# Optimization experiments

Hardware: AMD Instinct MI355X
Metric: run time of the kernel (lower is better)

Reference implementation:

```python
import jax, jax.numpy as jnp
import numpy as np

N_SAMPLES = 8388608  # total packed samples across all rays
N_RAYS = 131072      # number of rays (segments)


def setup_inputs() -> dict:
    key = jax.random.key(0)
    k1, k2, k3 = jax.random.split(key, 3)
    # Sorted segment ids emulate the packed ray layout (samples of a ray are contiguous).
    segment_ids = jnp.sort(
        jax.random.randint(k1, (N_SAMPLES,), 0, N_RAYS, dtype=jnp.int32)
    )
    rgb_samples = jax.random.normal(k2, (N_SAMPLES, 3), dtype=jnp.float32)
    weights_samples = jax.random.uniform(k3, (N_SAMPLES, 1), dtype=jnp.float32)
    return {
        "segment_ids": segment_ids,
        "rgb_samples": rgb_samples,
        "weights_samples": weights_samples,
        "n_rays": N_RAYS,
    }


def reference(segment_ids, rgb_samples, weights_samples, n_rays):
    # pred_rgb[r] = sum over samples s belonging to ray r of w_s * rgb_s
    weighted = rgb_samples * weights_samples  # [N,3], weight broadcast over channels
    pred_rgb = jax.ops.segment_sum(weighted, segment_ids, num_segments=n_rays)  # [n_rays,3]
    return pred_rgb
```

## Files before the change

kernel.cpp:

```cpp
#include <hip/hip_runtime.h>


__global__ __launch_bounds__(256) void find_starts_kernel(
    const int* __restrict__ ids, int n_samples, int n_rays,
    int* __restrict__ starts) {
  int i = blockIdx.x * blockDim.x + threadIdx.x;
  if (i >= n_samples) return;
  int b = ids[i];
  int a = (i == 0) ? -1 : ids[i - 1];
  for (int r = a + 1; r <= b; ++r) starts[r] = i;
  if (i == n_samples - 1) {
    for (int r = b + 1; r <= n_rays; ++r) starts[r] = n_samples;
  }
}

__global__ __launch_bounds__(256) void reduce_rays_kernel(
    const float* __restrict__ rgb, const float* __restrict__ w,
    const int* __restrict__ starts, float* __restrict__ out, int n_rays) {
  int gtid = blockIdx.x * blockDim.x + threadIdx.x;
  int ray = gtid >> 6;
  int lane = threadIdx.x & 63;
  if (ray >= n_rays) return;
  int s0 = starts[ray];
  int s1 = starts[ray + 1];
  float r = 0.f, g = 0.f, b = 0.f;
  for (int s = s0 + lane; s < s1; s += 64) {
    float ww = w[s];
    r += ww * rgb[3 * s + 0];
    g += ww * rgb[3 * s + 1];
    b += ww * rgb[3 * s + 2];
  }
  for (int off = 32; off; off >>= 1) {
    r += __shfl_down(r, off, 64);
    g += __shfl_down(g, off, 64);
    b += __shfl_down(b, off, 64);
  }
  if (lane == 0) {
    out[3 * ray + 0] = r;
    out[3 * ray + 1] = g;
    out[3 * ray + 2] = b;
  }
}

extern "C" void kernel_launch(void* const* d_in, const int* in_sizes, int n_in,
                              void* d_out, int out_size, void* d_ws, size_t ws_size,
                              hipStream_t stream) {
  const int*   segment_ids = (const int*)d_in[0];
  const float* rgb         = (const float*)d_in[1];
  const float* weights     = (const float*)d_in[2];
  float*       out         = (float*)d_out;

  const int n_samples = in_sizes[0];
  const int n_rays    = out_size / 3;

  int* starts = (int*)d_ws;

  {
    int threads = 256;
    int blocks = (n_samples + threads - 1) / threads;
    find_starts_kernel<<<blocks, threads, 0, stream>>>(
        segment_ids, n_samples, n_rays, starts);
  }
  {
    int threads = 256;
    long long total_threads = (long long)n_rays * 64;
    int blocks = (int)((total_threads + threads - 1) / threads);
    reduce_rays_kernel<<<blocks, threads, 0, stream>>>(
        rgb, weights, starts, out, n_rays);
  }
}
```

Measured before the change: 207.9 us.

## Vectorize boundary detection and coalesce RGB loads with shuffle-broadcast weights

find_starts now loads four segment ids per thread through int4 and takes the previous id from a neighbouring lane by warp shuffle. The reduction walks each ray's RGB data as a flat float stream, so consecutive lanes read consecutive floats instead of stride-3 addresses. Each lane's weight is broadcast to the matching channel lanes with __shfl, and lane%3 decides which accumulator belongs to which channel. The intent is fully coalesced loads in both kernels, at the cost of extra shuffles and slightly more involved channel bookkeeping.

```diff
diff --git a/kernel.cpp b/kernel.cpp
--- a/kernel.cpp
+++ b/kernel.cpp
@@ -4,41 +4,85 @@
 __global__ __launch_bounds__(256) void find_starts_kernel(
     const int* __restrict__ ids, int n_samples, int n_rays,
     int* __restrict__ starts) {
-  int i = blockIdx.x * blockDim.x + threadIdx.x;
-  if (i >= n_samples) return;
-  int b = ids[i];
-  int a = (i == 0) ? -1 : ids[i - 1];
-  for (int r = a + 1; r <= b; ++r) starts[r] = i;
-  if (i == n_samples - 1) {
-    for (int r = b + 1; r <= n_rays; ++r) starts[r] = n_samples;
+  int i4 = blockIdx.x * blockDim.x + threadIdx.x;
+  int base = i4 * 4;
+  if (base >= n_samples) return;
+  int lane = threadIdx.x & 63;
+
+  int4 v;
+  if (base + 3 < n_samples) {
+    v = ((const int4*)ids)[i4];
+  } else {
+    v.x = ids[base];
+    v.y = (base + 1 < n_samples) ? ids[base + 1] : v.x;
+    v.z = (base + 2 < n_samples) ? ids[base + 2] : v.y;
+    v.w = (base + 3 < n_samples) ? ids[base + 3] : v.z;
+  }
+  int prev = __shfl_up(v.w, 1, 64);
+  if (lane == 0) prev = (base == 0) ? -1 : ids[base - 1];
+
+  int a[5] = {prev, v.x, v.y, v.z, v.w};
+  #pragma unroll
+  for (int t = 0; t < 4; ++t) {
+    int hi = (base + t < n_samples) ? a[t + 1] : a[t];
+    for (int r = a[t] + 1; r <= hi; ++r) starts[r] = base + t;
+  }
+  if (base + 4 >= n_samples) {
+    int last = a[4];
+    for (int r = last + 1; r <= n_rays; ++r) starts[r] = n_samples;
   }
 }
 
 __global__ __launch_bounds__(256) void reduce_rays_kernel(
     const float* __restrict__ rgb, const float* __restrict__ w,
     const int* __restrict__ starts, float* __restrict__ out, int n_rays) {
-  int gtid = blockIdx.x * blockDim.x + threadIdx.x;
-  int ray = gtid >> 6;
   int lane = threadIdx.x & 63;
+  int ray = __builtin_amdgcn_readfirstlane(
+      blockIdx.x * (blockDim.x >> 6) + (threadIdx.x >> 6));
   if (ray >= n_rays) return;
   int s0 = starts[ray];
   int s1 = starts[ray + 1];
-  float r = 0.f, g = 0.f, b = 0.f;
-  for (int s = s0 + lane; s < s1; s += 64) {
-    float ww = w[s];
-    r += ww * rgb[3 * s + 0];
-    g += ww * rgb[3 * s + 1];
-    b += ww * rgb[3 * s + 2];
+  int L  = s1 - s0;
+  int nf = 3 * L;
+  const float* __restrict__ rgbf = rgb + 3 * (long long)s0;
+  const float* __restrict__ wseg = w + s0;
+
+  float acc0 = 0.f, acc1 = 0.f, acc2 = 0.f;
+  for (int k = 0; 192 * k < nf; ++k) {
+    int si = 64 * k + lane;
+    float wv = (si < L) ? wseg[si] : 0.f;
+    {
+      int e = 192 * k + lane;
+      float rv = (e < nf) ? rgbf[e] : 0.f;
+      acc0 += rv * __shfl(wv, lane / 3, 64);
+    }
+    {
+      int e = 192 * k + 64 + lane;
+      float rv = (e < nf) ? rgbf[e] : 0.f;
+      acc1 += rv * __shfl(wv, (64 + lane) / 3, 64);
+    }
+    {
+      int e = 192 * k + 128 + lane;
+      float rv = (e < nf) ? rgbf[e] : 0.f;
+      acc2 += rv * __shfl(wv, (128 + lane) / 3, 64);
+    }
   }
+
+  int m = lane % 3;
+  float c0 = (m == 0) ? acc0 : (m == 1) ? acc2 : acc1;
+  float c1 = (m == 0) ? acc1 : (m == 1) ? acc0 : acc2;
+  float c2 = (m == 0) ? acc2 : (m == 1) ? acc1 : acc0;
+
+  #pragma unroll
   for (int off = 32; off; off >>= 1) {
-    r += __shfl_down(r, off, 64);
-    g += __shfl_down(g, off, 64);
-    b += __shfl_down(b, off, 64);
+    c0 += __shfl_down(c0, off, 64);
+    c1 += __shfl_down(c1, off, 64);
+    c2 += __shfl_down(c2, off, 64);
   }
   if (lane == 0) {
-    out[3 * ray + 0] = r;
-    out[3 * ray + 1] = g;
-    out[3 * ray + 2] = b;
+    out[3 * ray + 0] = c0;
+    out[3 * ray + 1] = c1;
+    out[3 * ray + 2] = c2;
   }
 }
 
@@ -57,14 +101,14 @@
 
   {
     int threads = 256;
-    int blocks = (n_samples + threads - 1) / threads;
+    int elems4  = (n_samples + 3) / 4;
+    int blocks  = (elems4 + threads - 1) / threads;
     find_starts_kernel<<<blocks, threads, 0, stream>>>(
         segment_ids, n_samples, n_rays, starts);
   }
   {
     int threads = 256;
-    long long total_threads = (long long)n_rays * 64;
-    int blocks = (int)((total_threads + threads - 1) / threads);
+    int blocks  = (n_rays + 3) / 4;
     reduce_rays_kernel<<<blocks, threads, 0, stream>>>(
         rgb, weights, starts, out, n_rays);
   }
```

Measured after the change: 208.2 us. About the same (+0.1%).

## Replace start-index search and per-ray wave reduction with chunked LDS segmented accumulation

Applied to the files above, without the earlier changes.

Drops the two-pass scheme, which first built ray start offsets and then used one 64-lane wave per ray. Each block now processes a contiguous chunk of 1024 samples with vectorized float4 loads. Each thread merges runs of equal ids in registers, accumulates them into an LDS buffer with LDS atomics, and then writes interior rays directly and boundary rays with global atomics after a zeroing pass. This removes the starts workspace traffic and the poor lane utilization when rays hold only about 64 samples. In exchange it relies on float atomics, so summation order is nondeterministic, and it needs a separate kernel to zero the output. The leftover-element branch in the zeroing code is empty.

```diff
diff --git a/kernel.cpp b/kernel.cpp
--- a/kernel.cpp
+++ b/kernel.cpp
@@ -1,44 +1,125 @@
 #include <hip/hip_runtime.h>
 
 
-__global__ __launch_bounds__(256) void find_starts_kernel(
-    const int* __restrict__ ids, int n_samples, int n_rays,
-    int* __restrict__ starts) {
+#define CHUNK    1024
+#define CAP      1024
+#define NTHREADS 256
+
+__global__ __launch_bounds__(NTHREADS) void zero_out_kernel(float4* __restrict__ out4,
+                                                            int n4) {
   int i = blockIdx.x * blockDim.x + threadIdx.x;
-  if (i >= n_samples) return;
-  int b = ids[i];
-  int a = (i == 0) ? -1 : ids[i - 1];
-  for (int r = a + 1; r <= b; ++r) starts[r] = i;
-  if (i == n_samples - 1) {
-    for (int r = b + 1; r <= n_rays; ++r) starts[r] = n_samples;
-  }
+  if (i < n4) out4[i] = make_float4(0.f, 0.f, 0.f, 0.f);
 }
 
-__global__ __launch_bounds__(256) void reduce_rays_kernel(
-    const float* __restrict__ rgb, const float* __restrict__ w,
-    const int* __restrict__ starts, float* __restrict__ out, int n_rays) {
-  int gtid = blockIdx.x * blockDim.x + threadIdx.x;
-  int ray = gtid >> 6;
-  int lane = threadIdx.x & 63;
-  if (ray >= n_rays) return;
-  int s0 = starts[ray];
-  int s1 = starts[ray + 1];
-  float r = 0.f, g = 0.f, b = 0.f;
-  for (int s = s0 + lane; s < s1; s += 64) {
-    float ww = w[s];
-    r += ww * rgb[3 * s + 0];
-    g += ww * rgb[3 * s + 1];
-    b += ww * rgb[3 * s + 2];
+__global__ __launch_bounds__(NTHREADS) void integrate_kernel(
+    const int* __restrict__ ids, const float* __restrict__ rgb,
+    const float* __restrict__ w, float* __restrict__ out, int n_samples) {
+  __shared__ float acc[CAP * 3];
+  __shared__ int sh_first, sh_last, sh_leftc, sh_rightc;
+
+  const int block_start = blockIdx.x * CHUNK;
+  const int nproc = min(CHUNK, n_samples - block_start);
+
+  if (threadIdx.x == 0) {
+    int f = ids[block_start];
+    int l = ids[block_start + nproc - 1];
+    sh_first = f;
+    sh_last = l;
+    sh_leftc = (block_start == 0) || (ids[block_start - 1] != f);
+    sh_rightc = (block_start + nproc == n_samples) || (ids[block_start + nproc] != l);
   }
-  for (int off = 32; off; off >>= 1) {
-    r += __shfl_down(r, off, 64);
-    g += __shfl_down(g, off, 64);
-    b += __shfl_down(b, off, 64);
+  __syncthreads();
+  const int first = sh_first;
+  const int range = sh_last - first + 1;
+  const bool lds_path = (range <= CAP);
+
+  if (lds_path) {
+    for (int i = threadIdx.x; i < range * 3; i += NTHREADS) acc[i] = 0.f;
   }
-  if (lane == 0) {
-    out[3 * ray + 0] = r;
-    out[3 * ray + 1] = g;
-    out[3 * ray + 2] = b;
+  __syncthreads();
+
+  const int t0 = block_start + threadIdx.x * 4;
+  if (t0 < n_samples) {
+    int idv[4];
+    float px[4], py[4], pz[4];
+    if (t0 + 3 < n_samples) {
+      const int4 id4 = *(const int4*)(ids + t0);
+      const float4 w4 = *(const float4*)(w + t0);
+      const float4 r0 = *(const float4*)(rgb + 3 * t0);
+      const float4 r1 = *(const float4*)(rgb + 3 * t0 + 4);
+      const float4 r2 = *(const float4*)(rgb + 3 * t0 + 8);
+      idv[0] = id4.x; idv[1] = id4.y; idv[2] = id4.z; idv[3] = id4.w;
+      px[0] = r0.x * w4.x; py[0] = r0.y * w4.x; pz[0] = r0.z * w4.x;
+      px[1] = r0.w * w4.y; py[1] = r1.x * w4.y; pz[1] = r1.y * w4.y;
+      px[2] = r1.z * w4.z; py[2] = r1.w * w4.z; pz[2] = r2.x * w4.z;
+      px[3] = r2.y * w4.w; py[3] = r2.z * w4.w; pz[3] = r2.w * w4.w;
+    } else {
+      int cnt = n_samples - t0;
+      #pragma unroll
+      for (int j = 0; j < 4; ++j) {
+        if (j < cnt) {
+          idv[j] = ids[t0 + j];
+          float ww = w[t0 + j];
+          px[j] = rgb[3 * (t0 + j) + 0] * ww;
+          py[j] = rgb[3 * (t0 + j) + 1] * ww;
+          pz[j] = rgb[3 * (t0 + j) + 2] * ww;
+        } else {
+          idv[j] = idv[j - 1];
+          px[j] = py[j] = pz[j] = 0.f;
+        }
+      }
+    }
+
+    int runid = idv[0];
+    float rx = px[0], ry = py[0], rz = pz[0];
+    #pragma unroll
+    for (int j = 1; j < 4; ++j) {
+      if (idv[j] == runid) {
+        rx += px[j]; ry += py[j]; rz += pz[j];
+      } else {
+        if (lds_path) {
+          int b = 3 * (runid - first);
+          atomicAdd(&acc[b + 0], rx);
+          atomicAdd(&acc[b + 1], ry);
+          atomicAdd(&acc[b + 2], rz);
+        } else {
+          atomicAdd(&out[3 * runid + 0], rx);
+          atomicAdd(&out[3 * runid + 1], ry);
+          atomicAdd(&out[3 * runid + 2], rz);
+        }
+        runid = idv[j];
+        rx = px[j]; ry = py[j]; rz = pz[j];
+      }
+    }
+    if (lds_path) {
+      int b = 3 * (runid - first);
+      atomicAdd(&acc[b + 0], rx);
+      atomicAdd(&acc[b + 1], ry);
+      atomicAdd(&acc[b + 2], rz);
+    } else {
+      atomicAdd(&out[3 * runid + 0], rx);
+      atomicAdd(&out[3 * runid + 1], ry);
+      atomicAdd(&out[3 * runid + 2], rz);
+    }
+  }
+  __syncthreads();
+
+  if (lds_path) {
+    const bool lc = (bool)sh_leftc, rc = (bool)sh_rightc;
+    for (int rl = threadIdx.x; rl < range; rl += NTHREADS) {
+      int ray = first + rl;
+      float vx = acc[3 * rl + 0], vy = acc[3 * rl + 1], vz = acc[3 * rl + 2];
+      bool interior = (rl > 0 || lc) && (rl < range - 1 || rc);
+      if (interior) {
+        out[3 * ray + 0] = vx;
+        out[3 * ray + 1] = vy;
+        out[3 * ray + 2] = vz;
+      } else {
+        atomicAdd(&out[3 * ray + 0], vx);
+        atomicAdd(&out[3 * ray + 1], vy);
+        atomicAdd(&out[3 * ray + 2], vz);
+      }
+    }
   }
 }
 
@@ -51,21 +132,18 @@
   float*       out         = (float*)d_out;
 
   const int n_samples = in_sizes[0];
-  const int n_rays    = out_size / 3;
-
-  int* starts = (int*)d_ws;
 
   {
-    int threads = 256;
-    int blocks = (n_samples + threads - 1) / threads;
-    find_starts_kernel<<<blocks, threads, 0, stream>>>(
-        segment_ids, n_samples, n_rays, starts);
+    int n4 = out_size / 4;
+    int blocks = (n4 + NTHREADS - 1) / NTHREADS;
+    zero_out_kernel<<<blocks, NTHREADS, 0, stream>>>((float4*)out, n4);
+    int rem = out_size - n4 * 4;
+    if (rem > 0) {
+    }
   }
   {
-    int threads = 256;
-    long long total_threads = (long long)n_rays * 64;
-    int blocks = (int)((total_threads + threads - 1) / threads);
-    reduce_rays_kernel<<<blocks, threads, 0, stream>>>(
-        rgb, weights, starts, out, n_rays);
+    int blocks = (n_samples + CHUNK - 1) / CHUNK;
+    integrate_kernel<<<blocks, NTHREADS, 0, stream>>>(
+        segment_ids, rgb, weights, out, n_samples);
   }
 }
```

Result: faster. 202.9 us (-2.4%).

## Replace segment-start search with vectorized segmented wavefront scan plus atomics

Applied to the files above, without the earlier changes.

Drops the two-pass approach (build ray start offsets, then one 64-lane wavefront per ray) in favor of a single streaming pass. Each thread loads four samples with vector loads and combines runs of equal ids inside its registers. A segmented shuffle scan across the wavefront merges runs that span threads, and partial sums are written to the output with atomics after a zeroing kernel. This is meant to remove the poorly utilized per-ray wavefronts (rays average about 64 samples) and the starts array traffic. In exchange it adds atomic contention at segment boundaries and makes float summation order nondeterministic.

```diff
diff --git a/kernel.cpp b/kernel.cpp
--- a/kernel.cpp
+++ b/kernel.cpp
@@ -1,44 +1,110 @@
 #include <hip/hip_runtime.h>
 
 
-__global__ __launch_bounds__(256) void find_starts_kernel(
-    const int* __restrict__ ids, int n_samples, int n_rays,
-    int* __restrict__ starts) {
+#define NTHREADS 256
+
+__global__ __launch_bounds__(NTHREADS) void zero_out_kernel(float4* __restrict__ out4,
+                                                            int n4) {
   int i = blockIdx.x * blockDim.x + threadIdx.x;
-  if (i >= n_samples) return;
-  int b = ids[i];
-  int a = (i == 0) ? -1 : ids[i - 1];
-  for (int r = a + 1; r <= b; ++r) starts[r] = i;
-  if (i == n_samples - 1) {
-    for (int r = b + 1; r <= n_rays; ++r) starts[r] = n_samples;
-  }
+  if (i < n4) out4[i] = make_float4(0.f, 0.f, 0.f, 0.f);
 }
 
-__global__ __launch_bounds__(256) void reduce_rays_kernel(
-    const float* __restrict__ rgb, const float* __restrict__ w,
-    const int* __restrict__ starts, float* __restrict__ out, int n_rays) {
-  int gtid = blockIdx.x * blockDim.x + threadIdx.x;
-  int ray = gtid >> 6;
-  int lane = threadIdx.x & 63;
-  if (ray >= n_rays) return;
-  int s0 = starts[ray];
-  int s1 = starts[ray + 1];
-  float r = 0.f, g = 0.f, b = 0.f;
-  for (int s = s0 + lane; s < s1; s += 64) {
-    float ww = w[s];
-    r += ww * rgb[3 * s + 0];
-    g += ww * rgb[3 * s + 1];
-    b += ww * rgb[3 * s + 2];
+__global__ __launch_bounds__(NTHREADS) void integrate_kernel(
+    const int* __restrict__ ids, const float* __restrict__ rgb,
+    const float* __restrict__ w, float* __restrict__ out, int n_samples) {
+  const int lane = threadIdx.x & 63;
+  const long long t0 = (long long)(blockIdx.x * blockDim.x + threadIdx.x) * 4;
+
+  int idv[4];
+  float px[4], py[4], pz[4];
+  if (t0 + 3 < n_samples) {
+    const int4   id4 = *(const int4*)(ids + t0);
+    const float4 w4  = *(const float4*)(w + t0);
+    const float4 r0  = *(const float4*)(rgb + 3 * t0);
+    const float4 r1  = *(const float4*)(rgb + 3 * t0 + 4);
+    const float4 r2  = *(const float4*)(rgb + 3 * t0 + 8);
+    idv[0] = id4.x; idv[1] = id4.y; idv[2] = id4.z; idv[3] = id4.w;
+    px[0] = r0.x * w4.x; py[0] = r0.y * w4.x; pz[0] = r0.z * w4.x;
+    px[1] = r0.w * w4.y; py[1] = r1.x * w4.y; pz[1] = r1.y * w4.y;
+    px[2] = r1.z * w4.z; py[2] = r1.w * w4.z; pz[2] = r2.x * w4.z;
+    px[3] = r2.y * w4.w; py[3] = r2.z * w4.w; pz[3] = r2.w * w4.w;
+  } else {
+    int last = ids[n_samples - 1];
+    #pragma unroll
+    for (int j = 0; j < 4; ++j) {
+      long long s = t0 + j;
+      if (s < n_samples) {
+        idv[j] = ids[s];
+        float ww = w[s];
+        px[j] = rgb[3 * s + 0] * ww;
+        py[j] = rgb[3 * s + 1] * ww;
+        pz[j] = rgb[3 * s + 2] * ww;
+      } else {
+        idv[j] = (j == 0) ? last : idv[j - 1];
+        px[j] = py[j] = pz[j] = 0.f;
+      }
+    }
   }
-  for (int off = 32; off; off >>= 1) {
-    r += __shfl_down(r, off, 64);
-    g += __shfl_down(g, off, 64);
-    b += __shfl_down(b, off, 64);
+
+  const int id0 = idv[0], id3 = idv[3];
+  const bool f_intra = (id0 != id3);
+  const int hl = (idv[1] == id0) ? ((idv[2] == id0) ? ((idv[3] == id0) ? 4 : 3) : 2) : 1;
+  const int tl = (idv[2] == id3) ? ((idv[1] == id3) ? ((idv[0] == id3) ? 4 : 3) : 2) : 1;
+  float hx = 0.f, hy = 0.f, hz = 0.f, tx = 0.f, ty = 0.f, tz = 0.f;
+  #pragma unroll
+  for (int j = 0; j < 4; ++j) {
+    if (j < hl)     { hx += px[j]; hy += py[j]; hz += pz[j]; }
+    if (j >= 4 - tl){ tx += px[j]; ty += py[j]; tz += pz[j]; }
   }
-  if (lane == 0) {
-    out[3 * ray + 0] = r;
-    out[3 * ray + 1] = g;
-    out[3 * ray + 2] = b;
+  {
+    int ilo = hl, ihi = 3 - tl;
+    if (ilo <= ihi) {
+      if (ilo == ihi) {
+        atomicAdd(&out[3 * idv[ilo] + 0], px[ilo]);
+        atomicAdd(&out[3 * idv[ilo] + 1], py[ilo]);
+        atomicAdd(&out[3 * idv[ilo] + 2], pz[ilo]);
+      } else if (idv[ilo] == idv[ihi]) {
+        atomicAdd(&out[3 * idv[ilo] + 0], px[ilo] + px[ihi]);
+        atomicAdd(&out[3 * idv[ilo] + 1], py[ilo] + py[ihi]);
+        atomicAdd(&out[3 * idv[ilo] + 2], pz[ilo] + pz[ihi]);
+      } else {
+        atomicAdd(&out[3 * idv[ilo] + 0], px[ilo]);
+        atomicAdd(&out[3 * idv[ilo] + 1], py[ilo]);
+        atomicAdd(&out[3 * idv[ilo] + 2], pz[ilo]);
+        atomicAdd(&out[3 * idv[ihi] + 0], px[ihi]);
+        atomicAdd(&out[3 * idv[ihi] + 1], py[ihi]);
+        atomicAdd(&out[3 * idv[ihi] + 2], pz[ihi]);
+      }
+    }
+  }
+
+  const int prev_tid = __shfl_up(id3, 1, 64);
+  int fl = (lane == 0 || f_intra || prev_tid != id0) ? 1 : 0;
+  float sx = tx, sy = ty, sz = tz;
+  #pragma unroll
+  for (int off = 1; off < 64; off <<= 1) {
+    float ox = __shfl_up(sx, off, 64);
+    float oy = __shfl_up(sy, off, 64);
+    float oz = __shfl_up(sz, off, 64);
+    int  ofl = __shfl_up(fl, off, 64);
+    if (lane >= off && fl == 0) { sx += ox; sy += oy; sz += oz; fl = ofl; }
+  }
+
+  const float pSx = __shfl_up(sx, 1, 64);
+  const float pSy = __shfl_up(sy, 1, 64);
+  const float pSz = __shfl_up(sz, 1, 64);
+  if (f_intra) {
+    const bool link = (lane > 0) && (prev_tid == id0);
+    atomicAdd(&out[3 * id0 + 0], hx + (link ? pSx : 0.f));
+    atomicAdd(&out[3 * id0 + 1], hy + (link ? pSy : 0.f));
+    atomicAdd(&out[3 * id0 + 2], hz + (link ? pSz : 0.f));
+  }
+
+  const int next_hid = __shfl_down(id0, 1, 64);
+  if (lane == 63 || next_hid != id3) {
+    atomicAdd(&out[3 * id3 + 0], sx);
+    atomicAdd(&out[3 * id3 + 1], sy);
+    atomicAdd(&out[3 * id3 + 2], sz);
   }
 }
 
@@ -51,21 +117,16 @@
   float*       out         = (float*)d_out;
 
   const int n_samples = in_sizes[0];
-  const int n_rays    = out_size / 3;
-
-  int* starts = (int*)d_ws;
 
   {
-    int threads = 256;
-    int blocks = (n_samples + threads - 1) / threads;
-    find_starts_kernel<<<blocks, threads, 0, stream>>>(
-        segment_ids, n_samples, n_rays, starts);
+    int n4 = out_size / 4;
+    int blocks = (n4 + NTHREADS - 1) / NTHREADS;
+    zero_out_kernel<<<blocks, NTHREADS, 0, stream>>>((float4*)out, n4);
   }
   {
-    int threads = 256;
-    long long total_threads = (long long)n_rays * 64;
-    int blocks = (int)((total_threads + threads - 1) / threads);
-    reduce_rays_kernel<<<blocks, threads, 0, stream>>>(
-        rgb, weights, starts, out, n_rays);
+    int spb = NTHREADS * 4;
+    int blocks = (n_samples + spb - 1) / spb;
+    integrate_kernel<<<blocks, NTHREADS, 0, stream>>>(
+        segment_ids, rgb, weights, out, n_samples);
   }
 }
```

Result: faster. 194.6 us (-6.4%).
